# Performance work log

Measured on AMD Instinct MI355X. Metric: run time of the kernel, lower is better.

Reference implementation:

```python
import jax, jax.numpy as jnp
import numpy as np

B, S, D, H, L = 8, 1024, 512, 8, 6
DK = D // H
DFF = 4 * D
EPS = 1e-5
SCALE = float(np.sqrt(DK))  # torch: sqrt(d_k)


def setup_inputs() -> dict:
    key = jax.random.key(0)
    ks = jax.random.split(key, 10)
    init = lambda k, shape: jax.random.normal(k, shape, jnp.float32) * 0.02
    return {
        "x": jax.random.normal(ks[0], (B, S, D), jnp.float32),
        "qkv_w": init(ks[1], (L, D, 3 * D)),
        "qkv_b": init(ks[2], (L, 3 * D)),
        "out_w": init(ks[3], (L, D, D)),
        "out_b": init(ks[4], (L, D)),
        "ln1_g": jnp.ones((L, D), jnp.float32),
        "ln1_b": jnp.zeros((L, D), jnp.float32),
        "mlp_w1": init(ks[5], (L, D, DFF)),
        "mlp_b1": init(ks[6], (L, DFF)),
        "mlp_w2": init(ks[7], (L, DFF, D)),
        "mlp_b2": init(ks[8], (L, D)),
        "ln2_g": jnp.ones((L, D), jnp.float32),
        "ln2_b": jnp.zeros((L, D), jnp.float32),
    }


def _layer_norm(x, g, b):
    m = jnp.mean(x, axis=-1, keepdims=True)
    v = jnp.var(x, axis=-1, keepdims=True)  # biased var, matches torch LayerNorm
    return (x - m) * jax.lax.rsqrt(v + EPS) * g + b


def reference(x, qkv_w, qkv_b, out_w, out_b, ln1_g, ln1_b,
              mlp_w1, mlp_b1, mlp_w2, mlp_b2, ln2_g, ln2_b):
    b, s, d = x.shape
    causal = jnp.tril(jnp.ones((s, s), dtype=bool))  # [S,S]
    for i in range(L):
        # --- causal self-attention, post-LN residual (dropout = eval identity) ---
        qkv = x @ qkv_w[i] + qkv_b[i]                      # [B,S,3D]
        q, k, v = jnp.split(qkv, 3, axis=-1)
        q = q.reshape(b, s, H, DK)
        k = k.reshape(b, s, H, DK)
        v = v.reshape(b, s, H, DK)
        att = jnp.einsum('bqhd,bkhd->bhqk', q, k) / SCALE  # [B,H,S,S]
        att = jnp.where(causal, att, -jnp.inf)
        att = jax.nn.softmax(att, axis=-1)
        o = jnp.einsum('bhqk,bkhd->bqhd', att, v).reshape(b, s, d)
        x = _layer_norm(o @ out_w[i] + out_b[i] + x, ln1_g[i], ln1_b[i])
        # --- MLP, post-LN residual ---
        h = jax.nn.relu(x @ mlp_w1[i] + mlp_b1[i]) @ mlp_w2[i] + mlp_b2[i]
        x = _layer_norm(x + h, ln2_g[i], ln2_b[i])
    return x
```

## Files before the change

kernel.cpp:

```cpp
#include <hip/hip_runtime.h>
#include <math.h>

#define Bn   8
#define Sn   1024
#define Dn   512
#define Hn   8
#define DKn  64
#define Ln   6
#define DFFn 2048
#define Mn   (Bn * Sn)

typedef __bf16 bf16x8 __attribute__((ext_vector_type(8)));
typedef __bf16 bf16x4 __attribute__((ext_vector_type(4)));
typedef __bf16 bf16x2 __attribute__((ext_vector_type(2)));
typedef float  f32x4  __attribute__((ext_vector_type(4)));

__device__ __forceinline__ void gl_lds16(const void* g, void* l) {
    __builtin_amdgcn_global_load_lds(
        (const __attribute__((address_space(1))) void*)g,
        (__attribute__((address_space(3))) void*)l, 16, 0, 0);
}

__global__ __launch_bounds__(256) void k_cast_bf16(const float* __restrict__ in,
                                                   __bf16* __restrict__ out, int n) {
    int i = blockIdx.x * 256 + threadIdx.x;
    if (i < n) out[i] = (__bf16)in[i];
}

__global__ __launch_bounds__(256) void k_trans_all(
    const float* __restrict__ qkv_w, const float* __restrict__ out_w,
    const float* __restrict__ w1, const float* __restrict__ w2,
    __bf16* __restrict__ Wq, __bf16* __restrict__ Wo,
    __bf16* __restrict__ W1o, __bf16* __restrict__ W2o)
{
    const int lay = blockIdx.x / 3072;
    const int t   = blockIdx.x % 3072;
    const float* src; __bf16* dst; int K, N, n0, k0;
    if (t < 768)       { src = qkv_w + (size_t)lay * Dn * 3 * Dn; dst = Wq  + (size_t)lay * 3 * Dn * Dn;
                         K = 512;  N = 1536; int u = t;        n0 = (u % 48) * 32; k0 = (u / 48) * 32; }
    else if (t < 1024) { src = out_w + (size_t)lay * Dn * Dn;     dst = Wo  + (size_t)lay * Dn * Dn;
                         K = 512;  N = 512;  int u = t - 768;  n0 = (u % 16) * 32; k0 = (u / 16) * 32; }
    else if (t < 2048) { src = w1 + (size_t)lay * Dn * DFFn;      dst = W1o + (size_t)lay * DFFn * Dn;
                         K = 512;  N = 2048; int u = t - 1024; n0 = (u % 64) * 32; k0 = (u / 64) * 32; }
    else               { src = w2 + (size_t)lay * DFFn * Dn;      dst = W2o + (size_t)lay * Dn * DFFn;
                         K = 2048; N = 512;  int u = t - 2048; n0 = (u % 16) * 32; k0 = (u / 16) * 32; }

    __shared__ float tt[32][33];
    const int tx = threadIdx.x, ty = threadIdx.y;
    #pragma unroll
    for (int r = 0; r < 4; r++)
        tt[ty + 8 * r][tx] = src[(size_t)(k0 + ty + 8 * r) * N + n0 + tx];
    __syncthreads();
    #pragma unroll
    for (int r = 0; r < 4; r++)
        dst[(size_t)(n0 + ty + 8 * r) * K + k0 + tx] = (__bf16)tt[tx][ty + 8 * r];
}

template <int RELU, int OUTBF, int JT, int VW>
__global__ __launch_bounds__(256) void k_gemm_mfma(
    const __bf16* __restrict__ A, const __bf16* __restrict__ Bt,
    const float* __restrict__ bias, void* __restrict__ Cout,
    __bf16* __restrict__ Vt, int M, int N, int K, int NBX)
{
    constexpr int BN = JT * 32;
    __shared__ __bf16 As[128][64];
    __shared__ __bf16 Bs[BN][64];
    const int tid  = threadIdx.x;
    const int lane = tid & 63;
    const int wave = tid >> 6;
    const int wy   = wave >> 1, wx = wave & 1;
    const int m16  = lane & 15, quad = lane >> 4;

    const int cpx = gridDim.x >> 3;
    const int id  = (blockIdx.x & 7) * cpx + (blockIdx.x >> 3);
    const int bm  = (id / NBX) * 128;
    const int bn  = (id % NBX) * BN;

    f32x4 acc[4][JT];
    #pragma unroll
    for (int i = 0; i < 4; i++)
        #pragma unroll
        for (int j = 0; j < JT; j++)
            acc[i][j] = (f32x4){0.f, 0.f, 0.f, 0.f};

    const __bf16* Ap = A  + (size_t)bm * K;
    const __bf16* Bp = Bt + (size_t)bn * K;

    const int sw0 = ((quad    ) ^ (m16 & 7)) * 8;
    const int sw1 = ((quad + 4) ^ (m16 & 7)) * 8;

    for (int k0 = 0; k0 < K; k0 += 64) {
        __syncthreads();
        #pragma unroll
        for (int c = 0; c < 4; c++) {
            int lin = tid + c * 256;
            int row = lin >> 3, uu = lin & 7;
            int su  = (uu ^ (row & 7)) << 3;
            gl_lds16(Ap + (size_t)row * K + k0 + su, (void*)(&As[0][0] + lin * 8));
        }
        #pragma unroll
        for (int c = 0; c < JT; c++) {
            int lin = tid + c * 256;
            int row = lin >> 3, uu = lin & 7;
            int su  = (uu ^ (row & 7)) << 3;
            gl_lds16(Bp + (size_t)row * K + k0 + su, (void*)(&Bs[0][0] + lin * 8));
        }
        __syncthreads();

        bf16x8 af[4][2], bfr[JT][2];
        #pragma unroll
        for (int i = 0; i < 4; i++) {
            af[i][0] = *(const bf16x8*)&As[wy * 64 + i * 16 + m16][sw0];
            af[i][1] = *(const bf16x8*)&As[wy * 64 + i * 16 + m16][sw1];
        }
        #pragma unroll
        for (int j = 0; j < JT; j++) {
            bfr[j][0] = *(const bf16x8*)&Bs[wx * JT * 16 + j * 16 + m16][sw0];
            bfr[j][1] = *(const bf16x8*)&Bs[wx * JT * 16 + j * 16 + m16][sw1];
        }
        #pragma unroll
        for (int hc = 0; hc < 2; hc++)
            #pragma unroll
            for (int i = 0; i < 4; i++)
                #pragma unroll
                for (int j = 0; j < JT; j++)
                    acc[i][j] = __builtin_amdgcn_mfma_f32_16x16x32_bf16(
                        af[i][hc], bfr[j][hc], acc[i][j], 0, 0, 0);
    }

    float*  Cf = (float*)Cout;
    __bf16* Cb = (__bf16*)Cout;
    #pragma unroll
    for (int i = 0; i < 4; i++) {
        const int row0 = bm + wy * 64 + i * 16 + quad * 4;
        #pragma unroll
        for (int j = 0; j < JT; j++) {
            const int col = bn + wx * JT * 16 + j * 16 + m16;
            const float bv = bias[col];
            float vv[4];
            #pragma unroll
            for (int r = 0; r < 4; r++) {
                float v = acc[i][j][r] + bv;
                if (RELU) v = fmaxf(v, 0.f);
                vv[r] = v;
                if (OUTBF) Cb[(size_t)(row0 + r) * N + col] = (__bf16)v;
                else       Cf[(size_t)(row0 + r) * N + col] = v;
            }
            if (VW && col >= 1024) {
                const int cc = col - 1024;
                const int bb = row0 >> 10, ss = row0 & 1023;
                bf16x4 pv;
                #pragma unroll
                for (int r = 0; r < 4; r++) pv[r] = (__bf16)vv[r];
                *(bf16x4*)&Vt[((size_t)(bb * Hn + (cc >> 6)) * DKn + (cc & 63)) * Sn + ss] = pv;
            }
        }
    }
}

__device__ __forceinline__ void softmax_update(
    f32x4 sv[4], float m[4], float l[4], f32x4 acc[4],
    bool diag, int wave16, int quad, int m16,
    __bf16 (*Pw)[72], bf16x8& pf0, bf16x8& pf1)
{
    #pragma unroll
    for (int j = 0; j < 4; j++)
        #pragma unroll
        for (int r = 0; r < 4; r++) {
            float v = sv[j][r] * 0.125f;
            if (diag && (j * 16 + m16) > (wave16 + quad * 4 + r)) v = -1e30f;
            sv[j][r] = v;
        }

    float pm[4];
    #pragma unroll
    for (int r = 0; r < 4; r++)
        pm[r] = fmaxf(fmaxf(sv[0][r], sv[1][r]), fmaxf(sv[2][r], sv[3][r]));
    #pragma unroll
    for (int off = 1; off < 16; off <<= 1)
        #pragma unroll
        for (int r = 0; r < 4; r++)
            pm[r] = fmaxf(pm[r], __shfl_xor(pm[r], off, 16));

    bool grew = false;
    #pragma unroll
    for (int r = 0; r < 4; r++) grew = grew || (pm[r] > m[r] + 8.f);
    if (__any((int)grew)) {
        #pragma unroll
        for (int r = 0; r < 4; r++) {
            float mn = fmaxf(m[r], pm[r]);
            float al = __expf(m[r] - mn);
            m[r] = mn;
            l[r] *= al;
            #pragma unroll
            for (int j = 0; j < 4; j++) acc[j][r] *= al;
        }
    }

    float rs[4] = {0.f, 0.f, 0.f, 0.f};
    #pragma unroll
    for (int j = 0; j < 4; j++)
        #pragma unroll
        for (int r = 0; r < 4; r++) {
            float p = __expf(sv[j][r] - m[r]);
            rs[r] += p;
            Pw[quad * 4 + r][j * 16 + m16] = (__bf16)p;
        }
    #pragma unroll
    for (int off = 1; off < 16; off <<= 1)
        #pragma unroll
        for (int r = 0; r < 4; r++)
            rs[r] += __shfl_xor(rs[r], off, 16);
    #pragma unroll
    for (int r = 0; r < 4; r++) l[r] += rs[r];

    pf0 = *(const bf16x8*)&Pw[m16][quad * 8];
    pf1 = *(const bf16x8*)&Pw[m16][32 + quad * 8];
}

__global__ __launch_bounds__(512, 4) void k_attn_mfma(
    const __bf16* __restrict__ qkv, const __bf16* __restrict__ Vt,
    __bf16* __restrict__ o)
{
    const int id = blockIdx.x;
    const int pr = id >> 6;
    const int b  = (id >> 3) & 7;
    const int h  = id & 7;
    const int tid  = threadIdx.x;
    const int lane = tid & 63, wave = tid >> 6;
    const int m16  = lane & 15, quad = lane >> 4;
    const int isB  = wave >> 2;
    const int wave16 = (wave & 3) * 16;
    const int qtA  = pr, qtB = 15 - pr;
    const int qt   = isB ? qtB : qtA;

    __shared__ __bf16 Kb[2][64][64];
    __shared__ __bf16 Vb[2][64][64];
    __shared__ __bf16 Ps[8][16][72];

    const __bf16* base = qkv + (size_t)b * Sn * 1536 + h * DKn;
    const __bf16* vtb  = Vt + (size_t)(b * Hn + h) * DKn * Sn;
    __bf16 (*Pw)[72] = Ps[wave];

    const int sw0 = ((quad    ) ^ (m16 & 7)) * 8;
    const int sw1 = ((quad + 4) ^ (m16 & 7)) * 8;

    const int srow = tid >> 3;
    const int ssu  = ((tid & 7) ^ (srow & 7)) * 8;

    #define STAGE(KT, BB)                                                       \
        {                                                                       \
            gl_lds16(base + (size_t)((KT) * 64 + srow) * 1536 + 512 + ssu,      \
                     (void*)(&Kb[BB][0][0] + tid * 8));                         \
            gl_lds16(vtb + (size_t)srow * Sn + (KT) * 64 + ssu,                 \
                     (void*)(&Vb[BB][0][0] + tid * 8));                         \
        }

    STAGE(0, 0);

    bf16x8 q0, q1;
    {
        const __bf16* qa = base + (size_t)(qt * 64 + wave16 + m16) * 1536 + quad * 8;
        q0 = *(const bf16x8*)qa; q1 = *(const bf16x8*)(qa + 32);
    }

    float m[4], l[4];
    f32x4 acc[4];
    #pragma unroll
    for (int r = 0; r < 4; r++) {
        m[r] = -1e30f; l[r] = 0.f;
        acc[r] = (f32x4){0.f, 0.f, 0.f, 0.f};
    }

    __syncthreads();

    for (int kt = 0; kt <= qtB; kt++) {
        const int buf = kt & 1;
        if (kt < qtB) STAGE(kt + 1, buf ^ 1);

        if (isB || kt <= qtA) {
            f32x4 sv[4];
            __builtin_amdgcn_s_setprio(1);
            #pragma unroll
            for (int j = 0; j < 4; j++) {
                const int rk = j * 16 + m16;
                bf16x8 kf0 = *(const bf16x8*)&Kb[buf][rk][sw0];
                bf16x8 kf1 = *(const bf16x8*)&Kb[buf][rk][sw1];
                f32x4 s = (f32x4){0.f, 0.f, 0.f, 0.f};
                s = __builtin_amdgcn_mfma_f32_16x16x32_bf16(q0, kf0, s, 0, 0, 0);
                s = __builtin_amdgcn_mfma_f32_16x16x32_bf16(q1, kf1, s, 0, 0, 0);
                sv[j] = s;
            }
            __builtin_amdgcn_s_setprio(0);

            bf16x8 vf[4][2];
            #pragma unroll
            for (int jd = 0; jd < 4; jd++) {
                const int rv = jd * 16 + m16;
                vf[jd][0] = *(const bf16x8*)&Vb[buf][rv][sw0];
                vf[jd][1] = *(const bf16x8*)&Vb[buf][rv][sw1];
            }

            bf16x8 p0, p1;
            softmax_update(sv, m, l, acc, kt == qt, wave16, quad, m16, Pw, p0, p1);

            __builtin_amdgcn_s_setprio(1);
            #pragma unroll
            for (int jd = 0; jd < 4; jd++) {
                acc[jd] = __builtin_amdgcn_mfma_f32_16x16x32_bf16(p0, vf[jd][0], acc[jd], 0, 0, 0);
                acc[jd] = __builtin_amdgcn_mfma_f32_16x16x32_bf16(p1, vf[jd][1], acc[jd], 0, 0, 0);
            }
            __builtin_amdgcn_s_setprio(0);
        }

        __syncthreads();
    }
    #undef STAGE

    #pragma unroll
    for (int r = 0; r < 4; r++) l[r] = 1.0f / l[r];
    #pragma unroll
    for (int jd = 0; jd < 4; jd++)
        #pragma unroll
        for (int r = 0; r < 4; r++) {
            const int row = b * Sn + qt * 64 + wave16 + quad * 4 + r;
            o[(size_t)row * Dn + h * DKn + jd * 16 + m16] = (__bf16)(acc[jd][r] * l[r]);
        }
}

template <int FINAL>
__global__ __launch_bounds__(256) void k_residual_ln(
    const __bf16* __restrict__ t, __bf16* __restrict__ xb,
    const float* __restrict__ g, const float* __restrict__ be,
    float* __restrict__ outf)
{
    const int row  = (blockIdx.x << 2) | (threadIdx.x >> 6);
    const int lane = threadIdx.x & 63;
    const size_t base = (size_t)row * Dn + lane * 8;

    bf16x8 tv = *(const bf16x8*)&t[base];
    bf16x8 xv = *(const bf16x8*)&xb[base];
    float v[8];
    float s = 0.f;
    #pragma unroll
    for (int i = 0; i < 8; i++) {
        v[i] = (float)tv[i] + (float)xv[i];
        s += v[i];
    }
    #pragma unroll
    for (int off = 1; off < 64; off <<= 1) s += __shfl_xor(s, off);
    const float mean = s * (1.0f / Dn);

    float vs = 0.f;
    #pragma unroll
    for (int i = 0; i < 8; i++) {
        v[i] -= mean;
        vs += v[i] * v[i];
    }
    #pragma unroll
    for (int off = 1; off < 64; off <<= 1) vs += __shfl_xor(vs, off);
    const float inv = rsqrtf(vs * (1.0f / Dn) + 1e-5f);

    const f32x4 g0 = *(const f32x4*)&g[lane * 8];
    const f32x4 g1 = *(const f32x4*)&g[lane * 8 + 4];
    const f32x4 b0 = *(const f32x4*)&be[lane * 8];
    const f32x4 b1 = *(const f32x4*)&be[lane * 8 + 4];

    if (FINAL) {
        f32x4 o0, o1;
        #pragma unroll
        for (int i = 0; i < 4; i++) {
            o0[i] = v[i] * inv * g0[i] + b0[i];
            o1[i] = v[i + 4] * inv * g1[i] + b1[i];
        }
        *(f32x4*)&outf[base]     = o0;
        *(f32x4*)&outf[base + 4] = o1;
    } else {
        bf16x8 ov;
        #pragma unroll
        for (int i = 0; i < 4; i++) {
            ov[i]     = (__bf16)(v[i] * inv * g0[i] + b0[i]);
            ov[i + 4] = (__bf16)(v[i + 4] * inv * g1[i] + b1[i]);
        }
        *(bf16x8*)&xb[base] = ov;
    }
}

extern "C" void kernel_launch(void* const* d_in, const int* in_sizes, int n_in,
                              void* d_out, int out_size, void* d_ws, size_t ws_size,
                              hipStream_t stream)
{
    const float* x_in   = (const float*)d_in[0];
    const float* qkv_w  = (const float*)d_in[1];
    const float* qkv_b  = (const float*)d_in[2];
    const float* out_w  = (const float*)d_in[3];
    const float* out_b  = (const float*)d_in[4];
    const float* ln1_g  = (const float*)d_in[5];
    const float* ln1_b  = (const float*)d_in[6];
    const float* mlp_w1 = (const float*)d_in[7];
    const float* mlp_b1 = (const float*)d_in[8];
    const float* mlp_w2 = (const float*)d_in[9];
    const float* mlp_b2 = (const float*)d_in[10];
    const float* ln2_g  = (const float*)d_in[11];
    const float* ln2_b  = (const float*)d_in[12];

    char* p = (char*)d_ws;
    __bf16* Xb    = (__bf16*)p; p += (size_t)Mn * Dn * 2;
    __bf16* QKVb  = (__bf16*)p; p += (size_t)Mn * 3 * Dn * 2;
    __bf16* AOb   = (__bf16*)p; p += (size_t)Mn * Dn * 2;
    __bf16* Hb    = (__bf16*)p; p += (size_t)Mn * DFFn * 2;
    __bf16* BUF3b = (__bf16*)p; p += (size_t)Mn * Dn * 2;
    __bf16* Wq    = (__bf16*)p; p += (size_t)Ln * 3 * Dn * Dn * 2;
    __bf16* Wo    = (__bf16*)p; p += (size_t)Ln * Dn * Dn * 2;
    __bf16* W1    = (__bf16*)p; p += (size_t)Ln * DFFn * Dn * 2;
    __bf16* W2    = (__bf16*)p; p += (size_t)Ln * Dn * DFFn * 2;
    __bf16* Vt    = Hb;

    k_cast_bf16<<<(Mn * Dn) / 256, 256, 0, stream>>>(x_in, Xb, Mn * Dn);

    k_trans_all<<<Ln * 3072, dim3(32, 8), 0, stream>>>(
        qkv_w, out_w, mlp_w1, mlp_w2, Wq, Wo, W1, W2);

    for (int l = 0; l < Ln; l++) {
        const __bf16* Wql = Wq + (size_t)l * 3 * Dn * Dn;
        const __bf16* Wol = Wo + (size_t)l * Dn * Dn;
        const __bf16* W1l = W1 + (size_t)l * DFFn * Dn;
        const __bf16* W2l = W2 + (size_t)l * Dn * DFFn;

        k_gemm_mfma<0, 1, 4, 1><<<768, 256, 0, stream>>>(
            Xb, Wql, qkv_b + (size_t)l * 3 * Dn, QKVb, Vt, Mn, 3 * Dn, Dn, 12);
        k_attn_mfma<<<512, 512, 0, stream>>>(QKVb, Vt, AOb);
        k_gemm_mfma<0, 1, 2, 0><<<512, 256, 0, stream>>>(
            AOb, Wol, out_b + (size_t)l * Dn, BUF3b, nullptr, Mn, Dn, Dn, 8);
        k_residual_ln<0><<<Mn / 4, 256, 0, stream>>>(BUF3b, Xb,
            ln1_g + (size_t)l * Dn, ln1_b + (size_t)l * Dn, nullptr);
        k_gemm_mfma<1, 1, 4, 0><<<1024, 256, 0, stream>>>(
            Xb, W1l, mlp_b1 + (size_t)l * DFFn, Hb, nullptr, Mn, DFFn, Dn, 16);
        k_gemm_mfma<0, 1, 2, 0><<<512, 256, 0, stream>>>(
            Hb, W2l, mlp_b2 + (size_t)l * Dn, BUF3b, nullptr, Mn, Dn, DFFn, 8);
        if (l == Ln - 1)
            k_residual_ln<1><<<Mn / 4, 256, 0, stream>>>(BUF3b, Xb,
                ln2_g + (size_t)l * Dn, ln2_b + (size_t)l * Dn, (float*)d_out);
        else
            k_residual_ln<0><<<Mn / 4, 256, 0, stream>>>(BUF3b, Xb,
                ln2_g + (size_t)l * Dn, ln2_b + (size_t)l * Dn, nullptr);
    }
}
```

Baseline: 956.1 us.

## Parametrize GEMM K-tile and split attention into one query tile per block

The GEMM kernel gains a BK template parameter, and the two N=512 GEMMs (out-projection and MLP down-projection) now use a 128-wide K tile. This halves the number of barrier-separated k iterations and gives more MFMA work per sync, at the cost of twice the LDS per block. The attention kernel drops its paired-query-tile scheme (one 512-thread block handling tiles pr and 15-pr). It now launches 1024 blocks of 256 threads, each handling a single query tile, which removes idle waves in the shorter half but leaves the causal work unbalanced across blocks. Occupancy hints change from (512,4) to (256,3).

```diff
diff --git a/kernel.cpp b/kernel.cpp
--- a/kernel.cpp
+++ b/kernel.cpp
@@ -56,15 +56,17 @@
         dst[(size_t)(n0 + ty + 8 * r) * K + k0 + tx] = (__bf16)tt[tx][ty + 8 * r];
 }
 
-template <int RELU, int OUTBF, int JT, int VW>
+template <int RELU, int OUTBF, int JT, int VW, int BK>
 __global__ __launch_bounds__(256) void k_gemm_mfma(
     const __bf16* __restrict__ A, const __bf16* __restrict__ Bt,
     const float* __restrict__ bias, void* __restrict__ Cout,
     __bf16* __restrict__ Vt, int M, int N, int K, int NBX)
 {
     constexpr int BN = JT * 32;
-    __shared__ __bf16 As[128][64];
-    __shared__ __bf16 Bs[BN][64];
+    constexpr int UR = BK / 8;
+    constexpr int HC = BK / 32;
+    __shared__ __bf16 As[128][BK];
+    __shared__ __bf16 Bs[BN][BK];
     const int tid  = threadIdx.x;
     const int lane = tid & 63;
     const int wave = tid >> 6;
@@ -86,40 +88,42 @@
     const __bf16* Ap = A  + (size_t)bm * K;
     const __bf16* Bp = Bt + (size_t)bn * K;
 
-    const int sw0 = ((quad    ) ^ (m16 & 7)) * 8;
-    const int sw1 = ((quad + 4) ^ (m16 & 7)) * 8;
-
-    for (int k0 = 0; k0 < K; k0 += 64) {
+    int sw[HC];
+    #pragma unroll
+    for (int hc = 0; hc < HC; hc++)
+        sw[hc] = ((quad + 4 * hc) ^ (m16 & (UR - 1))) * 8;
+
+    for (int k0 = 0; k0 < K; k0 += BK) {
         __syncthreads();
         #pragma unroll
-        for (int c = 0; c < 4; c++) {
+        for (int c = 0; c < UR / 2; c++) {
             int lin = tid + c * 256;
-            int row = lin >> 3, uu = lin & 7;
-            int su  = (uu ^ (row & 7)) << 3;
+            int row = lin / UR, uu = lin % UR;
+            int su  = (uu ^ (row & (UR - 1))) << 3;
             gl_lds16(Ap + (size_t)row * K + k0 + su, (void*)(&As[0][0] + lin * 8));
         }
         #pragma unroll
-        for (int c = 0; c < JT; c++) {
+        for (int c = 0; c < (JT * UR) / 8; c++) {
             int lin = tid + c * 256;
-            int row = lin >> 3, uu = lin & 7;
-            int su  = (uu ^ (row & 7)) << 3;
+            int row = lin / UR, uu = lin % UR;
+            int su  = (uu ^ (row & (UR - 1))) << 3;
             gl_lds16(Bp + (size_t)row * K + k0 + su, (void*)(&Bs[0][0] + lin * 8));
         }
         __syncthreads();
 
-        bf16x8 af[4][2], bfr[JT][2];
-        #pragma unroll
-        for (int i = 0; i < 4; i++) {
-            af[i][0] = *(const bf16x8*)&As[wy * 64 + i * 16 + m16][sw0];
-            af[i][1] = *(const bf16x8*)&As[wy * 64 + i * 16 + m16][sw1];
-        }
-        #pragma unroll
-        for (int j = 0; j < JT; j++) {
-            bfr[j][0] = *(const bf16x8*)&Bs[wx * JT * 16 + j * 16 + m16][sw0];
-            bfr[j][1] = *(const bf16x8*)&Bs[wx * JT * 16 + j * 16 + m16][sw1];
-        }
-        #pragma unroll
-        for (int hc = 0; hc < 2; hc++)
+        bf16x8 af[4][HC], bfr[JT][HC];
+        #pragma unroll
+        for (int i = 0; i < 4; i++)
+            #pragma unroll
+            for (int hc = 0; hc < HC; hc++)
+                af[i][hc] = *(const bf16x8*)&As[wy * 64 + i * 16 + m16][sw[hc]];
+        #pragma unroll
+        for (int j = 0; j < JT; j++)
+            #pragma unroll
+            for (int hc = 0; hc < HC; hc++)
+                bfr[j][hc] = *(const bf16x8*)&Bs[wx * JT * 16 + j * 16 + m16][sw[hc]];
+        #pragma unroll
+        for (int hc = 0; hc < HC; hc++)
             #pragma unroll
             for (int i = 0; i < 4; i++)
                 #pragma unroll
@@ -218,25 +222,22 @@
     pf1 = *(const bf16x8*)&Pw[m16][32 + quad * 8];
 }
 
-__global__ __launch_bounds__(512, 4) void k_attn_mfma(
+__global__ __launch_bounds__(256, 3) void k_attn_mfma(
     const __bf16* __restrict__ qkv, const __bf16* __restrict__ Vt,
     __bf16* __restrict__ o)
 {
     const int id = blockIdx.x;
-    const int pr = id >> 6;
+    const int h  = id & 7;
     const int b  = (id >> 3) & 7;
-    const int h  = id & 7;
+    const int qt = id >> 6;
     const int tid  = threadIdx.x;
     const int lane = tid & 63, wave = tid >> 6;
     const int m16  = lane & 15, quad = lane >> 4;
-    const int isB  = wave >> 2;
-    const int wave16 = (wave & 3) * 16;
-    const int qtA  = pr, qtB = 15 - pr;
-    const int qt   = isB ? qtB : qtA;
+    const int wave16 = wave * 16;
 
     __shared__ __bf16 Kb[2][64][64];
     __shared__ __bf16 Vb[2][64][64];
-    __shared__ __bf16 Ps[8][16][72];
+    __shared__ __bf16 Ps[4][16][72];
 
     const __bf16* base = qkv + (size_t)b * Sn * 1536 + h * DKn;
     const __bf16* vtb  = Vt + (size_t)(b * Hn + h) * DKn * Sn;
@@ -245,15 +246,18 @@
     const int sw0 = ((quad    ) ^ (m16 & 7)) * 8;
     const int sw1 = ((quad + 4) ^ (m16 & 7)) * 8;
 
-    const int srow = tid >> 3;
-    const int ssu  = ((tid & 7) ^ (srow & 7)) * 8;
-
     #define STAGE(KT, BB)                                                       \
         {                                                                       \
-            gl_lds16(base + (size_t)((KT) * 64 + srow) * 1536 + 512 + ssu,      \
-                     (void*)(&Kb[BB][0][0] + tid * 8));                         \
-            gl_lds16(vtb + (size_t)srow * Sn + (KT) * 64 + ssu,                 \
-                     (void*)(&Vb[BB][0][0] + tid * 8));                         \
+            _Pragma("unroll")                                                   \
+            for (int c = 0; c < 2; c++) {                                       \
+                const int lin = tid + c * 256;                                  \
+                const int row = lin >> 3, uu = lin & 7;                         \
+                const int su  = (uu ^ (row & 7)) * 8;                           \
+                gl_lds16(base + (size_t)((KT) * 64 + row) * 1536 + 512 + su,    \
+                         (void*)(&Kb[BB][0][0] + lin * 8));                     \
+                gl_lds16(vtb + (size_t)row * Sn + (KT) * 64 + su,               \
+                         (void*)(&Vb[BB][0][0] + lin * 8));                     \
+            }                                                                   \
         }
 
     STAGE(0, 0);
@@ -274,44 +278,42 @@
 
     __syncthreads();
 
-    for (int kt = 0; kt <= qtB; kt++) {
+    for (int kt = 0; kt <= qt; kt++) {
         const int buf = kt & 1;
-        if (kt < qtB) STAGE(kt + 1, buf ^ 1);
-
-        if (isB || kt <= qtA) {
-            f32x4 sv[4];
-            __builtin_amdgcn_s_setprio(1);
-            #pragma unroll
-            for (int j = 0; j < 4; j++) {
-                const int rk = j * 16 + m16;
-                bf16x8 kf0 = *(const bf16x8*)&Kb[buf][rk][sw0];
-                bf16x8 kf1 = *(const bf16x8*)&Kb[buf][rk][sw1];
-                f32x4 s = (f32x4){0.f, 0.f, 0.f, 0.f};
-                s = __builtin_amdgcn_mfma_f32_16x16x32_bf16(q0, kf0, s, 0, 0, 0);
-                s = __builtin_amdgcn_mfma_f32_16x16x32_bf16(q1, kf1, s, 0, 0, 0);
-                sv[j] = s;
-            }
-            __builtin_amdgcn_s_setprio(0);
-
-            bf16x8 vf[4][2];
-            #pragma unroll
-            for (int jd = 0; jd < 4; jd++) {
-                const int rv = jd * 16 + m16;
-                vf[jd][0] = *(const bf16x8*)&Vb[buf][rv][sw0];
-                vf[jd][1] = *(const bf16x8*)&Vb[buf][rv][sw1];
-            }
-
-            bf16x8 p0, p1;
-            softmax_update(sv, m, l, acc, kt == qt, wave16, quad, m16, Pw, p0, p1);
-
-            __builtin_amdgcn_s_setprio(1);
-            #pragma unroll
-            for (int jd = 0; jd < 4; jd++) {
-                acc[jd] = __builtin_amdgcn_mfma_f32_16x16x32_bf16(p0, vf[jd][0], acc[jd], 0, 0, 0);
-                acc[jd] = __builtin_amdgcn_mfma_f32_16x16x32_bf16(p1, vf[jd][1], acc[jd], 0, 0, 0);
-            }
-            __builtin_amdgcn_s_setprio(0);
-        }
+        if (kt < qt) STAGE(kt + 1, buf ^ 1);
+
+        f32x4 sv[4];
+        __builtin_amdgcn_s_setprio(1);
+        #pragma unroll
+        for (int j = 0; j < 4; j++) {
+            const int rk = j * 16 + m16;
+            bf16x8 kf0 = *(const bf16x8*)&Kb[buf][rk][sw0];
+            bf16x8 kf1 = *(const bf16x8*)&Kb[buf][rk][sw1];
+            f32x4 s = (f32x4){0.f, 0.f, 0.f, 0.f};
+            s = __builtin_amdgcn_mfma_f32_16x16x32_bf16(q0, kf0, s, 0, 0, 0);
+            s = __builtin_amdgcn_mfma_f32_16x16x32_bf16(q1, kf1, s, 0, 0, 0);
+            sv[j] = s;
+        }
+        __builtin_amdgcn_s_setprio(0);
+
+        bf16x8 vf[4][2];
+        #pragma unroll
+        for (int jd = 0; jd < 4; jd++) {
+            const int rv = jd * 16 + m16;
+            vf[jd][0] = *(const bf16x8*)&Vb[buf][rv][sw0];
+            vf[jd][1] = *(const bf16x8*)&Vb[buf][rv][sw1];
+        }
+
+        bf16x8 p0, p1;
+        softmax_update(sv, m, l, acc, kt == qt, wave16, quad, m16, Pw, p0, p1);
+
+        __builtin_amdgcn_s_setprio(1);
+        #pragma unroll
+        for (int jd = 0; jd < 4; jd++) {
+            acc[jd] = __builtin_amdgcn_mfma_f32_16x16x32_bf16(p0, vf[jd][0], acc[jd], 0, 0, 0);
+            acc[jd] = __builtin_amdgcn_mfma_f32_16x16x32_bf16(p1, vf[jd][1], acc[jd], 0, 0, 0);
+        }
+        __builtin_amdgcn_s_setprio(0);
 
         __syncthreads();
     }
@@ -427,16 +429,16 @@
         const __bf16* W1l = W1 + (size_t)l * DFFn * Dn;
         const __bf16* W2l = W2 + (size_t)l * Dn * DFFn;
 
-        k_gemm_mfma<0, 1, 4, 1><<<768, 256, 0, stream>>>(
+        k_gemm_mfma<0, 1, 4, 1, 64><<<768, 256, 0, stream>>>(
             Xb, Wql, qkv_b + (size_t)l * 3 * Dn, QKVb, Vt, Mn, 3 * Dn, Dn, 12);
-        k_attn_mfma<<<512, 512, 0, stream>>>(QKVb, Vt, AOb);
-        k_gemm_mfma<0, 1, 2, 0><<<512, 256, 0, stream>>>(
+        k_attn_mfma<<<1024, 256, 0, stream>>>(QKVb, Vt, AOb);
+        k_gemm_mfma<0, 1, 2, 0, 128><<<512, 256, 0, stream>>>(
             AOb, Wol, out_b + (size_t)l * Dn, BUF3b, nullptr, Mn, Dn, Dn, 8);
         k_residual_ln<0><<<Mn / 4, 256, 0, stream>>>(BUF3b, Xb,
             ln1_g + (size_t)l * Dn, ln1_b + (size_t)l * Dn, nullptr);
-        k_gemm_mfma<1, 1, 4, 0><<<1024, 256, 0, stream>>>(
+        k_gemm_mfma<1, 1, 4, 0, 64><<<1024, 256, 0, stream>>>(
             Xb, W1l, mlp_b1 + (size_t)l * DFFn, Hb, nullptr, Mn, DFFn, Dn, 16);
-        k_gemm_mfma<0, 1, 2, 0><<<512, 256, 0, stream>>>(
+        k_gemm_mfma<0, 1, 2, 0, 128><<<512, 256, 0, stream>>>(
             Hb, W2l, mlp_b2 + (size_t)l * Dn, BUF3b, nullptr, Mn, Dn, DFFn, 8);
         if (l == Ln - 1)
             k_residual_ln<1><<<Mn / 4, 256, 0, stream>>>(BUF3b, Xb,
```

Measured after the change: 956.1 us. About the same (-0.0%).
